# Optimization experiments

Hardware: AMD Instinct MI355X
Metric: run time of the kernel (lower is better)

Reference implementation:

```python
import jax, jax.numpy as jnp
import numpy as np

N, M, FEAT, GROUP, EMB = 512, 4096, 1024, 16, 64
DIM_GROUP = FEAT // GROUP  # 64


def _make_boxes(key, n):
    k1, k2, k3, k4 = jax.random.split(key, 4)
    cx = jax.random.uniform(k1, (n,), minval=0.0, maxval=800.0)
    cy = jax.random.uniform(k2, (n,), minval=0.0, maxval=800.0)
    w = jax.random.uniform(k3, (n,), minval=16.0, maxval=256.0)
    h = jax.random.uniform(k4, (n,), minval=16.0, maxval=256.0)
    return jnp.stack([cx - 0.5 * w, cy - 0.5 * h, cx + 0.5 * w, cy + 0.5 * h], axis=1)


def setup_inputs() -> dict:
    key = jax.random.key(0)
    ks = jax.random.split(key, 10)
    return {
        "roi_feat": jax.random.normal(ks[0], (N, FEAT), dtype=jnp.float32),
        "ref_feat": jax.random.normal(ks[1], (M, FEAT), dtype=jnp.float32),
        "rois_cur": _make_boxes(ks[2], N),
        "rois_ref": _make_boxes(ks[3], M),
        "Wg_w": jax.random.normal(ks[4], (GROUP, EMB), dtype=jnp.float32) * 0.01,
        "Wg_b": jnp.zeros((GROUP,), dtype=jnp.float32),
        "Wq_w": jax.random.normal(ks[5], (FEAT, FEAT), dtype=jnp.float32) * (1.0 / np.sqrt(FEAT)),
        "Wq_b": jnp.zeros((FEAT,), dtype=jnp.float32),
        "Wk_w": jax.random.normal(ks[6], (FEAT, FEAT), dtype=jnp.float32) * (1.0 / np.sqrt(FEAT)),
        "Wk_b": jnp.zeros((FEAT,), dtype=jnp.float32),
        "Wv_w": jax.random.normal(ks[7], (FEAT, FEAT), dtype=jnp.float32) * 0.01,  # grouped 1x1 conv: [16 groups x 64 out, 1024 in-per-group]
        "Wv_b": jnp.zeros((FEAT,), dtype=jnp.float32),
    }


def _position_embedding(bbox, ref_bbox):
    # extract_position_matrix
    xmin, ymin, xmax, ymax = [ref_bbox[:, i] for i in range(4)]
    w_ref = xmax - xmin + 1.0
    h_ref = ymax - ymin + 1.0
    cx_ref = 0.5 * (xmin + xmax)
    cy_ref = 0.5 * (ymin + ymax)
    xmin, ymin, xmax, ymax = [bbox[:, i] for i in range(4)]
    w = xmax - xmin + 1.0
    h = ymax - ymin + 1.0
    cx = 0.5 * (xmin + xmax)
    cy = 0.5 * (ymin + ymax)
    dx = jnp.log(jnp.abs((cx[:, None] - cx_ref[None, :]) / w[:, None]) + 0.001)
    dy = jnp.log(jnp.abs((cy[:, None] - cy_ref[None, :]) / h[:, None]) + 0.001)
    dw = jnp.log(w[:, None] / w_ref[None, :])
    dh = jnp.log(h[:, None] / h_ref[None, :])
    pos = jnp.stack([dx, dy, dw, dh], axis=2)  # [N, M, 4]
    # extract_position_embedding with feat_dim=64, wave_length=1000
    feat_range = jnp.arange(EMB // 8, dtype=jnp.float32)  # 8
    dim_mat = jnp.power(1000.0, (8.0 / EMB) * feat_range)  # [8]
    div = (pos * 100.0)[..., None] / dim_mat  # [N, M, 4, 8]
    emb = jnp.concatenate([jnp.sin(div), jnp.cos(div)], axis=3)  # [N, M, 4, 16]
    return emb.reshape(pos.shape[0], pos.shape[1], EMB)  # [N, M, 64]


def reference(roi_feat, ref_feat, rois_cur, rois_ref,
              Wg_w, Wg_b, Wq_w, Wq_b, Wk_w, Wk_b, Wv_w, Wv_b):
    emb = _position_embedding(rois_cur, rois_ref)  # [N, M, 64]
    # Wg: 1x1 conv over embedding channels -> per-group bias [N, G, M]
    aff_weight = jax.nn.relu(jnp.einsum('nme,ge->ngm', emb, Wg_w) + Wg_b[None, :, None])
    q = (roi_feat @ Wq_w.T + Wq_b).reshape(-1, GROUP, DIM_GROUP)  # [N, G, dg]
    k = (ref_feat @ Wk_w.T + Wk_b).reshape(-1, GROUP, DIM_GROUP)  # [M, G, dg]
    aff_scale = jnp.einsum('ngd,mgd->ngm', q, k) * (1.0 / np.sqrt(DIM_GROUP))
    weighted_aff = jnp.log(aff_weight + 1e-6) + aff_scale
    aff_softmax = jax.nn.softmax(weighted_aff, axis=2)  # [N, G, M]
    out_t = jnp.einsum('ngm,mf->ngf', aff_softmax, ref_feat)  # [N, G, FEAT]
    # grouped 1x1 conv Wv: group g maps its FEAT inputs to DIM_GROUP outputs
    Wv_g = Wv_w.reshape(GROUP, DIM_GROUP, FEAT)
    output = jnp.einsum('ngf,gof->ngo', out_t, Wv_g).reshape(-1, FEAT) + Wv_b
    return output
```

## Files before the change

kernel.cpp:

```cpp
#include <hip/hip_runtime.h>
#include <hip/hip_bf16.h>

#define N_ROI 512
#define M_REF 4096
#define FEAT 1024
#define GROUP 16
#define DG 64
#define EMB 64
#define GLDH 72
#define MSPLIT 32
#define MRANGE (M_REF / MSPLIT)
#define MCHUNK 64
#define BP2 72
#define DEFER_THR 8.0f

using f16x8 = __attribute__((ext_vector_type(8))) _Float16;
using f16x4 = __attribute__((ext_vector_type(4))) _Float16;
using f32x4 = __attribute__((ext_vector_type(4))) float;

__global__ __launch_bounds__(256) void cast_f16_5(
    const float* __restrict__ s0, _Float16* __restrict__ d0, int n0,
    const float* __restrict__ s1, _Float16* __restrict__ d1, int n1,
    const float* __restrict__ s2, _Float16* __restrict__ d2, int n2,
    const float* __restrict__ s3, _Float16* __restrict__ d3, int n3,
    const float* __restrict__ s4, _Float16* __restrict__ d4, int n4) {
  const int q0 = n0 >> 2, q1 = n1 >> 2, q2 = n2 >> 2, q3 = n3 >> 2, q4 = n4 >> 2;
  const int total = q0 + q1 + q2 + q3 + q4;
  for (int i = blockIdx.x * 256 + threadIdx.x; i < total;
       i += gridDim.x * 256) {
    int j = i;
    const float* s;
    _Float16* d;
    if (j < q0) { s = s0; d = d0; }
    else { j -= q0;
      if (j < q1) { s = s1; d = d1; }
      else { j -= q1;
        if (j < q2) { s = s2; d = d2; }
        else { j -= q2;
          if (j < q3) { s = s3; d = d3; }
          else { j -= q3; s = s4; d = d4; } } } }
    float4 v = *(const float4*)&s[(size_t)j * 4];
    *(f16x4*)&d[(size_t)j * 4] =
        f16x4{(_Float16)v.x, (_Float16)v.y, (_Float16)v.z, (_Float16)v.w};
  }
}

__global__ __launch_bounds__(256) void gemm_ff16(
    const _Float16* __restrict__ A, const _Float16* __restrict__ B,
    const float* __restrict__ bias, _Float16* __restrict__ C,
    int M, int N, int K) {
  __shared__ _Float16 As[128 * GLDH];
  __shared__ _Float16 Bs[64 * GLDH];
  const int tid = threadIdx.x, lane = tid & 63, wid = tid >> 6;
  const int bm = blockIdx.y * 128, bn = blockIdx.x * 64;
  const int wr = (wid >> 1) * 64, wc = (wid & 1) * 32;
  const int lrow = lane & 15, lk = (lane >> 4) * 8;

  f16x8 ra[4], rb[2];
#pragma unroll
  for (int i = 0; i < 4; ++i) {
    int idx = tid + i * 256, r = idx >> 3, c = (idx & 7) * 8;
    ra[i] = *(const f16x8*)&A[(size_t)(bm + r) * K + c];
  }
#pragma unroll
  for (int i = 0; i < 2; ++i) {
    int idx = tid + i * 256, r = idx >> 3, c = (idx & 7) * 8;
    rb[i] = *(const f16x8*)&B[(size_t)(bn + r) * K + c];
  }

  f32x4 acc[4][2] = {};
  for (int k0 = 0; k0 < K; k0 += 64) {
#pragma unroll
    for (int i = 0; i < 4; ++i) {
      int idx = tid + i * 256, r = idx >> 3, c = (idx & 7) * 8;
      *(f16x8*)&As[r * GLDH + c] = ra[i];
    }
#pragma unroll
    for (int i = 0; i < 2; ++i) {
      int idx = tid + i * 256, r = idx >> 3, c = (idx & 7) * 8;
      *(f16x8*)&Bs[r * GLDH + c] = rb[i];
    }
    __syncthreads();
    if (k0 + 64 < K) {
#pragma unroll
      for (int i = 0; i < 4; ++i) {
        int idx = tid + i * 256, r = idx >> 3, c = (idx & 7) * 8;
        ra[i] = *(const f16x8*)&A[(size_t)(bm + r) * K + k0 + 64 + c];
      }
#pragma unroll
      for (int i = 0; i < 2; ++i) {
        int idx = tid + i * 256, r = idx >> 3, c = (idx & 7) * 8;
        rb[i] = *(const f16x8*)&B[(size_t)(bn + r) * K + k0 + 64 + c];
      }
    }
    f16x8 a[4][2], b[2][2];
#pragma unroll
    for (int mi = 0; mi < 4; ++mi)
#pragma unroll
      for (int ks = 0; ks < 2; ++ks)
        a[mi][ks] = *(const f16x8*)&As[(wr + mi * 16 + lrow) * GLDH + ks * 32 + lk];
#pragma unroll
    for (int ni = 0; ni < 2; ++ni)
#pragma unroll
      for (int ks = 0; ks < 2; ++ks)
        b[ni][ks] = *(const f16x8*)&Bs[(wc + ni * 16 + lrow) * GLDH + ks * 32 + lk];
#pragma unroll
    for (int ks = 0; ks < 2; ++ks)
#pragma unroll
      for (int mi = 0; mi < 4; ++mi)
#pragma unroll
        for (int ni = 0; ni < 2; ++ni)
          acc[mi][ni] = __builtin_amdgcn_mfma_f32_16x16x32_f16(
              a[mi][ks], b[ni][ks], acc[mi][ni], 0, 0, 0);
    __syncthreads();
  }
#pragma unroll
  for (int mi = 0; mi < 4; ++mi)
#pragma unroll
    for (int ni = 0; ni < 2; ++ni) {
      int col = bn + wc + ni * 16 + lrow;
      float bv = bias ? bias[col] : 0.0f;
#pragma unroll
      for (int i = 0; i < 4; ++i) {
        int row = bm + wr + mi * 16 + (lane >> 4) * 4 + i;
        C[(size_t)row * N + col] = (_Float16)(acc[mi][ni][i] + bv);
      }
    }
}

__global__ __launch_bounds__(512) void attn_fused_kernel(
    const float* __restrict__ rois_cur, const float* __restrict__ rois_ref,
    const float* __restrict__ Wg_w, const float* __restrict__ Wg_b,
    const _Float16* __restrict__ q, const _Float16* __restrict__ k,
    const _Float16* __restrict__ vt, _Float16* __restrict__ pacc,
    float* __restrict__ pml) {
  __shared__ _Float16 Bias[GROUP][16][BP2];
  const int tid = threadIdx.x, lane = tid & 63, w = tid >> 6;
  const int bid = blockIdx.x;
  const int split = bid & (MSPLIT - 1), nt = bid >> 5;
  const int n0 = nt * 16;
  const int mb0 = split * MRANGE;
  const int lm = lane & 15, lc = lane >> 4;
  const int g0 = w * 2;
  const int mq = w & 3;
  const int nh = (w >> 2) * 8;

  f16x8 wgf[2];
#pragma unroll
  for (int kc = 0; kc < 2; ++kc) {
    const float* p = Wg_w + lm * EMB + kc * 32 + lc * 8;
#pragma unroll
    for (int j = 0; j < 8; ++j) wgf[kc][j] = (_Float16)p[j];
  }
  float wgb[4];
#pragma unroll
  for (int i = 0; i < 4; ++i) wgb[i] = Wg_b[lc * 4 + i];

  f16x8 qb[2][2];
#pragma unroll
  for (int gi = 0; gi < 2; ++gi)
#pragma unroll
    for (int kc = 0; kc < 2; ++kc)
      qb[gi][kc] = *(const f16x8*)
          &q[(size_t)(n0 + lm) * FEAT + (g0 + gi) * DG + kc * 32 + lc * 8];

  f32x4 acc[2][4] = {};
  float mrun[2] = {-1e30f, -1e30f}, lrun[2] = {0.0f, 0.0f};

  const float inv_dim[8] = {1.0f,          0.42169651f,  0.17782794f,
                            0.074989417f,  0.031622776f, 0.013335214f,
                            0.0056234133f, 0.0023713737f};
  const int isY = lc >> 1;
  const int useCos = lc & 1;

  for (int ch = 0; ch < MRANGE / MCHUNK; ++ch) {
    const int cb = mb0 + ch * MCHUNK;
    const int mglob = cb + mq * 16 + lm;

    const float4 rb = reinterpret_cast<const float4*>(rois_ref)[mglob];
    const float wr_ = rb.z - rb.x + 1.0f, hr_ = rb.w - rb.y + 1.0f;
    const float cxr = 0.5f * (rb.x + rb.z), cyr = 0.5f * (rb.y + rb.w);
    const float lwr = __logf(wr_), lhr = __logf(hr_);

    __syncthreads();

    for (int nl = nh; nl < nh + 8; ++nl) {
      const int n = n0 + nl;
      const float x0 = rois_cur[n * 4 + 0], y0 = rois_cur[n * 4 + 1];
      const float x1 = rois_cur[n * 4 + 2], y1 = rois_cur[n * 4 + 3];
      const float ww = x1 - x0 + 1.0f, hh = y1 - y0 + 1.0f;
      const float cx = 0.5f * (x0 + x1), cy = 0.5f * (y0 + y1);
      float pa, pb;
      if (isY) {
        pa = __logf(fabsf((cy - cyr) / hh) + 0.001f);
        pb = __logf(hh) - lhr;
      } else {
        pa = __logf(fabsf((cx - cxr) / ww) + 0.001f);
        pb = __logf(ww) - lwr;
      }
      pa *= 100.0f;
      pb *= 100.0f;
      f16x8 ef0, ef1;
#pragma unroll
      for (int f = 0; f < 8; ++f) {
        const float xa = pa * inv_dim[f];
        const float xb = pb * inv_dim[f];
        ef0[f] = (_Float16)(useCos ? __cosf(xa) : __sinf(xa));
        ef1[f] = (_Float16)(useCos ? __cosf(xb) : __sinf(xb));
      }
      f32x4 bacc = {};
      bacc = __builtin_amdgcn_mfma_f32_16x16x32_f16(wgf[0], ef0, bacc, 0, 0, 0);
      bacc = __builtin_amdgcn_mfma_f32_16x16x32_f16(wgf[1], ef1, bacc, 0, 0, 0);
#pragma unroll
      for (int i = 0; i < 4; ++i) {
        float v = fmaxf(bacc[i] + wgb[i], 0.0f);
        Bias[lc * 4 + i][nl][mq * 16 + lm] = (_Float16)__logf(v + 1e-6f);
      }
    }
    __syncthreads();

    for (int st = 0; st < 2; ++st) {
      const int ms = cb + st * 32;
#pragma unroll
      for (int gi = 0; gi < 2; ++gi) {
        const int g = g0 + gi;
        const size_t kbase = (size_t)(ms + lm) * FEAT + g * DG + lc * 8;
        f16x8 ka0a = *(const f16x8*)&k[kbase];
        f16x8 ka0b = *(const f16x8*)&k[kbase + 32];
        f16x8 ka1a = *(const f16x8*)&k[kbase + (size_t)16 * FEAT];
        f16x8 ka1b = *(const f16x8*)&k[kbase + (size_t)16 * FEAT + 32];
        f32x4 sAa = {}, sBa = {};
        sAa = __builtin_amdgcn_mfma_f32_16x16x32_f16(ka0a, qb[gi][0], sAa, 0, 0, 0);
        sAa = __builtin_amdgcn_mfma_f32_16x16x32_f16(ka0b, qb[gi][1], sAa, 0, 0, 0);
        sBa = __builtin_amdgcn_mfma_f32_16x16x32_f16(ka1a, qb[gi][0], sBa, 0, 0, 0);
        sBa = __builtin_amdgcn_mfma_f32_16x16x32_f16(ka1b, qb[gi][1], sBa, 0, 0, 0);
        const f16x4 bA = *(const f16x4*)&Bias[g][lm][st * 32 + lc * 4];
        const f16x4 bB = *(const f16x4*)&Bias[g][lm][st * 32 + 16 + lc * 4];
        float s[8];
#pragma unroll
        for (int i = 0; i < 4; ++i) {
          s[i] = (float)bA[i] + sAa[i] * 0.125f;
          s[4 + i] = (float)bB[i] + sBa[i] * 0.125f;
        }
        float cmax = s[0];
#pragma unroll
        for (int i = 1; i < 8; ++i) cmax = fmaxf(cmax, s[i]);
        cmax = fmaxf(cmax, __shfl_xor(cmax, 16));
        cmax = fmaxf(cmax, __shfl_xor(cmax, 32));
        if (!__all(cmax <= mrun[gi] + DEFER_THR)) {
          const float mnew = fmaxf(mrun[gi], cmax);
          const float fac = __expf(mrun[gi] - mnew);
          lrun[gi] *= fac;
#pragma unroll
          for (int ct = 0; ct < 4; ++ct)
#pragma unroll
            for (int i = 0; i < 4; ++i) acc[gi][ct][i] *= fac;
          mrun[gi] = mnew;
        }
        float p[8];
        float csum = 0.0f;
#pragma unroll
        for (int i = 0; i < 8; ++i) {
          p[i] = __expf(s[i] - mrun[gi]);
          csum += p[i];
        }
        csum += __shfl_xor(csum, 16);
        csum += __shfl_xor(csum, 32);
        lrun[gi] += csum;
        f16x8 pfrag;
#pragma unroll
        for (int j = 0; j < 8; ++j) pfrag[j] = (_Float16)p[j];
#pragma unroll
        for (int ct = 0; ct < 4; ++ct) {
          const size_t vrow = (size_t)(g * DG + ct * 16 + lm) * M_REF + ms;
          const f16x4 vA = *(const f16x4*)&vt[vrow + lc * 4];
          const f16x4 vB = *(const f16x4*)&vt[vrow + 16 + lc * 4];
          const f16x8 vf = {vA[0], vA[1], vA[2], vA[3],
                            vB[0], vB[1], vB[2], vB[3]};
          acc[gi][ct] = __builtin_amdgcn_mfma_f32_16x16x32_f16(vf, pfrag,
                                                              acc[gi][ct], 0, 0, 0);
        }
      }
    }
  }

#pragma unroll
  for (int gi = 0; gi < 2; ++gi) {
    const size_t base = (size_t)(nt * GROUP + g0 + gi) * MSPLIT + split;
#pragma unroll
    for (int ct = 0; ct < 4; ++ct) {
      f16x4 h = {(_Float16)acc[gi][ct][0], (_Float16)acc[gi][ct][1],
                 (_Float16)acc[gi][ct][2], (_Float16)acc[gi][ct][3]};
      *(f16x4*)&pacc[(base * 16 + lm) * 64 + ct * 16 + lc * 4] = h;
    }
    if (lc == 0) {
      pml[(base * 16 + lm) * 2 + 0] = mrun[gi];
      pml[(base * 16 + lm) * 2 + 1] = lrun[gi];
    }
  }
}

__global__ __launch_bounds__(256) void combine_kernel(
    const _Float16* __restrict__ pacc, const float* __restrict__ pml,
    const float* __restrict__ Wv_b, float* __restrict__ out) {
  const int nt = blockIdx.x >> 4, g = blockIdx.x & 15;
  const int r = threadIdx.x >> 4, c0 = (threadIdx.x & 15) * 4;
  const size_t gb = (size_t)(nt * GROUP + g) * MSPLIT;

  float ms[MSPLIT];
  float M = -1e30f;
#pragma unroll
  for (int s = 0; s < MSPLIT; ++s) {
    ms[s] = pml[((gb + s) * 16 + r) * 2 + 0];
    M = fmaxf(M, ms[s]);
  }
  float D = 0.0f;
  float4 o = {0.0f, 0.0f, 0.0f, 0.0f};
  float* po = &o.x;
#pragma unroll
  for (int s = 0; s < MSPLIT; ++s) {
    const float e = __expf(ms[s] - M);
    D += e * pml[((gb + s) * 16 + r) * 2 + 1];
    const f16x4 a = *(const f16x4*)&pacc[((gb + s) * 16 + r) * 64 + c0];
    po[0] += e * (float)a[0];
    po[1] += e * (float)a[1];
    po[2] += e * (float)a[2];
    po[3] += e * (float)a[3];
  }
  const float inv = 1.0f / D;
#pragma unroll
  for (int j = 0; j < 4; ++j)
    po[j] = po[j] * inv + Wv_b[g * DG + c0 + j];
  *(float4*)&out[(size_t)(nt * 16 + r) * FEAT + g * DG + c0] = o;
}

extern "C" void kernel_launch(void* const* d_in, const int* in_sizes, int n_in,
                              void* d_out, int out_size, void* d_ws,
                              size_t ws_size, hipStream_t stream) {
  const float* roi_feat = (const float*)d_in[0];
  const float* ref_feat = (const float*)d_in[1];
  const float* rois_cur = (const float*)d_in[2];
  const float* rois_ref = (const float*)d_in[3];
  const float* Wg_w = (const float*)d_in[4];
  const float* Wg_b = (const float*)d_in[5];
  const float* Wq_w = (const float*)d_in[6];
  const float* Wq_b = (const float*)d_in[7];
  const float* Wk_w = (const float*)d_in[8];
  const float* Wk_b = (const float*)d_in[9];
  const float* Wv_w = (const float*)d_in[10];
  const float* Wv_b = (const float*)d_in[11];
  float* out = (float*)d_out;

  _Float16* q16 = (_Float16*)d_ws;
  _Float16* k16 = q16 + (size_t)N_ROI * FEAT;
  _Float16* vt16 = k16 + (size_t)M_REF * FEAT;
  _Float16* roi16 = vt16 + (size_t)FEAT * M_REF;
  _Float16* ref16 = roi16 + (size_t)N_ROI * FEAT;
  _Float16* wq16 = ref16 + (size_t)M_REF * FEAT;
  _Float16* wk16 = wq16 + (size_t)FEAT * FEAT;
  _Float16* wv16 = wk16 + (size_t)FEAT * FEAT;
  _Float16* pacc = wv16 + (size_t)FEAT * FEAT;
  float* pml = (float*)(pacc + (size_t)N_ROI * GROUP * MSPLIT * 64);

  cast_f16_5<<<dim3(2048), 256, 0, stream>>>(
      roi_feat, roi16, N_ROI * FEAT, ref_feat, ref16, M_REF * FEAT,
      Wq_w, wq16, FEAT * FEAT, Wk_w, wk16, FEAT * FEAT,
      Wv_w, wv16, FEAT * FEAT);

  gemm_ff16<<<dim3(FEAT / 64, N_ROI / 128), 256, 0, stream>>>(
      roi16, wq16, Wq_b, q16, N_ROI, FEAT, FEAT);
  gemm_ff16<<<dim3(FEAT / 64, M_REF / 128), 256, 0, stream>>>(
      ref16, wk16, Wk_b, k16, M_REF, FEAT, FEAT);
  gemm_ff16<<<dim3(M_REF / 64, FEAT / 128), 256, 0, stream>>>(
      wv16, ref16, nullptr, vt16, FEAT, M_REF, FEAT);

  attn_fused_kernel<<<dim3((N_ROI / 16) * MSPLIT), 512, 0, stream>>>(
      rois_cur, rois_ref, Wg_w, Wg_b, q16, k16, vt16, pacc, pml);

  combine_kernel<<<dim3((N_ROI / 16) * GROUP), 256, 0, stream>>>(
      pacc, pml, Wv_b, out);
}
```

Baseline: 278.4 us.

## Double-buffer position bias tiles and permute V columns for single vector loads

```diff
diff --git a/kernel.cpp b/kernel.cpp
--- a/kernel.cpp
+++ b/kernel.cpp
@@ -10,8 +10,8 @@
 #define GLDH 72
 #define MSPLIT 32
 #define MRANGE (M_REF / MSPLIT)
-#define MCHUNK 64
-#define BP2 72
+#define NCH (MRANGE / 32)
+#define BPAD 36
 #define DEFER_THR 8.0f
 
 using f16x8 = __attribute__((ext_vector_type(8))) _Float16;
@@ -45,6 +45,7 @@
   }
 }
 
+template <bool PERM>
 __global__ __launch_bounds__(256) void gemm_ff16(
     const _Float16* __restrict__ A, const _Float16* __restrict__ B,
     const float* __restrict__ bias, _Float16* __restrict__ C,
@@ -120,6 +121,12 @@
     for (int ni = 0; ni < 2; ++ni) {
       int col = bn + wc + ni * 16 + lrow;
       float bv = bias ? bias[col] : 0.0f;
+      if (PERM) {
+        const int co = col & 31;
+        const int cp = (co < 16) ? ((co >> 2) * 8 + (co & 3))
+                                 : (((co & 15) >> 2) * 8 + 4 + (co & 3));
+        col = (col & ~31) | cp;
+      }
 #pragma unroll
       for (int i = 0; i < 4; ++i) {
         int row = bm + wr + mi * 16 + (lane >> 4) * 4 + i;
@@ -134,7 +141,7 @@
     const _Float16* __restrict__ q, const _Float16* __restrict__ k,
     const _Float16* __restrict__ vt, _Float16* __restrict__ pacc,
     float* __restrict__ pml) {
-  __shared__ _Float16 Bias[GROUP][16][BP2];
+  __shared__ _Float16 Bias[2][GROUP][16][BPAD];
   const int tid = threadIdx.x, lane = tid & 63, w = tid >> 6;
   const int bid = blockIdx.x;
   const int split = bid & (MSPLIT - 1), nt = bid >> 5;
@@ -142,8 +149,8 @@
   const int mb0 = split * MRANGE;
   const int lm = lane & 15, lc = lane >> 4;
   const int g0 = w * 2;
-  const int mq = w & 3;
-  const int nh = (w >> 2) * 8;
+  const int mt = w & 1;
+  const int nb = (w >> 1) * 4;
 
   f16x8 wgf[2];
 #pragma unroll
@@ -173,18 +180,14 @@
   const int isY = lc >> 1;
   const int useCos = lc & 1;
 
-  for (int ch = 0; ch < MRANGE / MCHUNK; ++ch) {
-    const int cb = mb0 + ch * MCHUNK;
-    const int mglob = cb + mq * 16 + lm;
-
-    const float4 rb = reinterpret_cast<const float4*>(rois_ref)[mglob];
+  auto produce = [&](int cc, int buf) {
+    const int mg = mb0 + cc * 32 + mt * 16 + lm;
+    const float4 rb = reinterpret_cast<const float4*>(rois_ref)[mg];
     const float wr_ = rb.z - rb.x + 1.0f, hr_ = rb.w - rb.y + 1.0f;
     const float cxr = 0.5f * (rb.x + rb.z), cyr = 0.5f * (rb.y + rb.w);
     const float lwr = __logf(wr_), lhr = __logf(hr_);
-
-    __syncthreads();
-
-    for (int nl = nh; nl < nh + 8; ++nl) {
+#pragma unroll
+    for (int nl = nb; nl < nb + 4; ++nl) {
       const int n = n0 + nl;
       const float x0 = rois_cur[n * 4 + 0], y0 = rois_cur[n * 4 + 1];
       const float x1 = rois_cur[n * 4 + 2], y1 = rois_cur[n * 4 + 3];
@@ -214,74 +217,77 @@
 #pragma unroll
       for (int i = 0; i < 4; ++i) {
         float v = fmaxf(bacc[i] + wgb[i], 0.0f);
-        Bias[lc * 4 + i][nl][mq * 16 + lm] = (_Float16)__logf(v + 1e-6f);
+        Bias[buf][lc * 4 + i][nl][mt * 16 + lm] = (_Float16)__logf(v + 1e-6f);
+      }
+    }
+  };
+
+  produce(0, 0);
+  __syncthreads();
+
+  for (int c = 0; c < NCH; ++c) {
+    const int cb = mb0 + c * 32;
+    const int cbuf = c & 1;
+    if (c + 1 < NCH) produce(c + 1, cbuf ^ 1);
+
+#pragma unroll
+    for (int gi = 0; gi < 2; ++gi) {
+      const int g = g0 + gi;
+      const size_t kbase = (size_t)(cb + lm) * FEAT + g * DG + lc * 8;
+      f16x8 ka0a = *(const f16x8*)&k[kbase];
+      f16x8 ka0b = *(const f16x8*)&k[kbase + 32];
+      f16x8 ka1a = *(const f16x8*)&k[kbase + (size_t)16 * FEAT];
+      f16x8 ka1b = *(const f16x8*)&k[kbase + (size_t)16 * FEAT + 32];
+      f32x4 sAa = {}, sBa = {};
+      sAa = __builtin_amdgcn_mfma_f32_16x16x32_f16(ka0a, qb[gi][0], sAa, 0, 0, 0);
+      sAa = __builtin_amdgcn_mfma_f32_16x16x32_f16(ka0b, qb[gi][1], sAa, 0, 0, 0);
+      sBa = __builtin_amdgcn_mfma_f32_16x16x32_f16(ka1a, qb[gi][0], sBa, 0, 0, 0);
+      sBa = __builtin_amdgcn_mfma_f32_16x16x32_f16(ka1b, qb[gi][1], sBa, 0, 0, 0);
+      const f16x4 bA = *(const f16x4*)&Bias[cbuf][g][lm][lc * 4];
+      const f16x4 bB = *(const f16x4*)&Bias[cbuf][g][lm][16 + lc * 4];
+      float s[8];
+#pragma unroll
+      for (int i = 0; i < 4; ++i) {
+        s[i] = (float)bA[i] + sAa[i] * 0.125f;
+        s[4 + i] = (float)bB[i] + sBa[i] * 0.125f;
+      }
+      float cmax = s[0];
+#pragma unroll
+      for (int i = 1; i < 8; ++i) cmax = fmaxf(cmax, s[i]);
+      cmax = fmaxf(cmax, __shfl_xor(cmax, 16));
+      cmax = fmaxf(cmax, __shfl_xor(cmax, 32));
+      if (!__all(cmax <= mrun[gi] + DEFER_THR)) {
+        const float mnew = fmaxf(mrun[gi], cmax);
+        const float fac = __expf(mrun[gi] - mnew);
+        lrun[gi] *= fac;
+#pragma unroll
+        for (int ct = 0; ct < 4; ++ct)
+#pragma unroll
+          for (int i = 0; i < 4; ++i) acc[gi][ct][i] *= fac;
+        mrun[gi] = mnew;
+      }
+      float p[8];
+      float csum = 0.0f;
+#pragma unroll
+      for (int i = 0; i < 8; ++i) {
+        p[i] = __expf(s[i] - mrun[gi]);
+        csum += p[i];
+      }
+      csum += __shfl_xor(csum, 16);
+      csum += __shfl_xor(csum, 32);
+      lrun[gi] += csum;
+      f16x8 pfrag;
+#pragma unroll
+      for (int j = 0; j < 8; ++j) pfrag[j] = (_Float16)p[j];
+#pragma unroll
+      for (int ct = 0; ct < 4; ++ct) {
+        const f16x8 vf = *(const f16x8*)
+            &vt[(size_t)(g * DG + ct * 16 + lm) * M_REF + cb + lc * 8];
+        acc[gi][ct] = __builtin_amdgcn_mfma_f32_16x16x32_f16(vf, pfrag,
+                                                            acc[gi][ct], 0, 0, 0);
       }
     }
     __syncthreads();
-
-    for (int st = 0; st < 2; ++st) {
-      const int ms = cb + st * 32;
-#pragma unroll
-      for (int gi = 0; gi < 2; ++gi) {
-        const int g = g0 + gi;
-        const size_t kbase = (size_t)(ms + lm) * FEAT + g * DG + lc * 8;
-        f16x8 ka0a = *(const f16x8*)&k[kbase];
-        f16x8 ka0b = *(const f16x8*)&k[kbase + 32];
-        f16x8 ka1a = *(const f16x8*)&k[kbase + (size_t)16 * FEAT];
-        f16x8 ka1b = *(const f16x8*)&k[kbase + (size_t)16 * FEAT + 32];
-        f32x4 sAa = {}, sBa = {};
-        sAa = __builtin_amdgcn_mfma_f32_16x16x32_f16(ka0a, qb[gi][0], sAa, 0, 0, 0);
-        sAa = __builtin_amdgcn_mfma_f32_16x16x32_f16(ka0b, qb[gi][1], sAa, 0, 0, 0);
-        sBa = __builtin_amdgcn_mfma_f32_16x16x32_f16(ka1a, qb[gi][0], sBa, 0, 0, 0);
-        sBa = __builtin_amdgcn_mfma_f32_16x16x32_f16(ka1b, qb[gi][1], sBa, 0, 0, 0);
-        const f16x4 bA = *(const f16x4*)&Bias[g][lm][st * 32 + lc * 4];
-        const f16x4 bB = *(const f16x4*)&Bias[g][lm][st * 32 + 16 + lc * 4];
-        float s[8];
-#pragma unroll
-        for (int i = 0; i < 4; ++i) {
-          s[i] = (float)bA[i] + sAa[i] * 0.125f;
-          s[4 + i] = (float)bB[i] + sBa[i] * 0.125f;
-        }
-        float cmax = s[0];
-#pragma unroll
-        for (int i = 1; i < 8; ++i) cmax = fmaxf(cmax, s[i]);
-        cmax = fmaxf(cmax, __shfl_xor(cmax, 16));
-        cmax = fmaxf(cmax, __shfl_xor(cmax, 32));
-        if (!__all(cmax <= mrun[gi] + DEFER_THR)) {
-          const float mnew = fmaxf(mrun[gi], cmax);
-          const float fac = __expf(mrun[gi] - mnew);
-          lrun[gi] *= fac;
-#pragma unroll
-          for (int ct = 0; ct < 4; ++ct)
-#pragma unroll
-            for (int i = 0; i < 4; ++i) acc[gi][ct][i] *= fac;
-          mrun[gi] = mnew;
-        }
-        float p[8];
-        float csum = 0.0f;
-#pragma unroll
-        for (int i = 0; i < 8; ++i) {
-          p[i] = __expf(s[i] - mrun[gi]);
-          csum += p[i];
-        }
-        csum += __shfl_xor(csum, 16);
-        csum += __shfl_xor(csum, 32);
-        lrun[gi] += csum;
-        f16x8 pfrag;
-#pragma unroll
-        for (int j = 0; j < 8; ++j) pfrag[j] = (_Float16)p[j];
-#pragma unroll
-        for (int ct = 0; ct < 4; ++ct) {
-          const size_t vrow = (size_t)(g * DG + ct * 16 + lm) * M_REF + ms;
-          const f16x4 vA = *(const f16x4*)&vt[vrow + lc * 4];
-          const f16x4 vB = *(const f16x4*)&vt[vrow + 16 + lc * 4];
-          const f16x8 vf = {vA[0], vA[1], vA[2], vA[3],
-                            vB[0], vB[1], vB[2], vB[3]};
-          acc[gi][ct] = __builtin_amdgcn_mfma_f32_16x16x32_f16(vf, pfrag,
-                                                              acc[gi][ct], 0, 0, 0);
-        }
-      }
-    }
   }
 
 #pragma unroll
@@ -367,11 +373,11 @@
       Wq_w, wq16, FEAT * FEAT, Wk_w, wk16, FEAT * FEAT,
       Wv_w, wv16, FEAT * FEAT);
 
-  gemm_ff16<<<dim3(FEAT / 64, N_ROI / 128), 256, 0, stream>>>(
+  gemm_ff16<false><<<dim3(FEAT / 64, N_ROI / 128), 256, 0, stream>>>(
       roi16, wq16, Wq_b, q16, N_ROI, FEAT, FEAT);
-  gemm_ff16<<<dim3(FEAT / 64, M_REF / 128), 256, 0, stream>>>(
+  gemm_ff16<false><<<dim3(FEAT / 64, M_REF / 128), 256, 0, stream>>>(
       ref16, wk16, Wk_b, k16, M_REF, FEAT, FEAT);
-  gemm_ff16<<<dim3(M_REF / 64, FEAT / 128), 256, 0, stream>>>(
+  gemm_ff16<true><<<dim3(M_REF / 64, FEAT / 128), 256, 0, stream>>>(
       wv16, ref16, nullptr, vt16, FEAT, M_REF, FEAT);
 
   attn_fused_kernel<<<dim3((N_ROI / 16) * MSPLIT), 512, 0, stream>>>(
```

Result: faster. 261.7 us (-6.0%).
